# Kernel optimization log

Hardware: AMD Instinct MI355X
Metric: run time of the kernel (lower is better)

Reference implementation:

```python
import jax, jax.numpy as jnp
import numpy as np

N_NODES = 50000
N_EDGES = 1000000
IN_F = 128
OUT_F = 128
K = 4
NEG_SLOPE = 0.01  # torch nn.LeakyReLU() default
EPS = 1e-8


def setup_inputs() -> dict:
    key = jax.random.key(0)
    k1, k2, k3, k4, k5, k6 = jax.random.split(key, 6)
    x = jax.random.normal(k1, (N_NODES, IN_F), dtype=jnp.float32)
    e = jax.random.uniform(k2, (N_NODES, K), dtype=jnp.float32)
    stdv = 1.0 / np.sqrt(OUT_F)
    weights = jax.random.uniform(k3, (K, IN_F, OUT_F), minval=-stdv, maxval=stdv, dtype=jnp.float32)
    a = jax.random.normal(k4, (K, 2 * OUT_F, 1), dtype=jnp.float32) * 0.1
    # edge_index with no self-loops (remove_self_loops is then a no-op)
    row = jax.random.randint(k5, (N_EDGES,), 0, N_NODES)
    off = jax.random.randint(k6, (N_EDGES,), 1, N_NODES)
    col = (row + off) % N_NODES
    adj = jnp.stack([row, col]).astype(jnp.int64)
    return {"x": x, "e": e, "weights": weights, "a": a, "adj": adj}


def _canet_gat_forward(x, e, weights, a, adj):
    N = x.shape[0]
    out_f = weights.shape[-1]
    # add self loops (input has none)
    loops = jnp.arange(N, dtype=adj.dtype)
    src = jnp.concatenate([adj[0], loops])  # [Et]
    dst = jnp.concatenate([adj[1], loops])  # [Et]

    # per-head projection: [K, N, O]
    h = jnp.einsum('nd,kdo->kno', x, weights)

    # attention logits: a = [a_src; a_dst], logit_e = leakyrelu(h[src].a_src + h[dst].a_dst)
    a_src = a[:, :out_f, 0]   # [K, O]
    a_dst = a[:, out_f:, 0]   # [K, O]
    s_src = jnp.einsum('kno,ko->kn', h, a_src)  # [K, N]
    s_dst = jnp.einsum('kno,ko->kn', h, a_dst)  # [K, N]
    logits = s_src[:, src] + s_dst[:, dst]      # [K, Et]
    logits = jnp.where(logits >= 0, logits, NEG_SLOPE * logits)
    logits_max = jnp.max(logits, axis=1, keepdims=True)  # global max per head
    edge_e = jnp.exp(logits - logits_max)                # [K, Et]

    outputs = []
    for k in range(h.shape[0]):  # small fixed loop over heads (avoids [K,Et,O] blowup)
        denom = jax.ops.segment_sum(edge_e[k], src, num_segments=N) + EPS   # [N]
        msg = edge_e[k][:, None] * h[k][dst]                                # [Et, O]
        hi_k = jax.ops.segment_sum(msg, src, num_segments=N)                # [N, O]
        outputs.append(hi_k / denom[:, None])
    outputs = jnp.stack(outputs, axis=1)  # [N, K, O]

    out = jnp.sum(e[:, :, None] * outputs, axis=1)  # [N, O]
    return out + x  # residual (in_features == out_features)


def reference(x, e, weights, a, adj):
    return _canet_gat_forward(x, e, weights, a, adj)
```

## Files before the change

kernel.cpp:

```cpp
#include <hip/hip_runtime.h>
#include <hip/hip_bf16.h>
#include <cstddef>

#define NN 50000
#define NE 1000000
#define F  128
#define KH 4
#define NEG 0.01f
#define EPSF 1e-8f
#define CAP 64
#define NBIN 196
#define BINCAP 8192
#define EPB 4096
#define NB1 ((NE + EPB - 1) / EPB)
#define NBW 256
#define NBP 1024

typedef short bf16x8 __attribute__((ext_vector_type(8)));
typedef float f32x4 __attribute__((ext_vector_type(4)));

__device__ inline ushort f2bf(float f) {
    __hip_bfloat16 b = __float2bfloat16(f);
    return *reinterpret_cast<ushort*>(&b);
}
__device__ inline float2 bf2_to_f2(unsigned int v) {
    union { unsigned int u; float f; } a, b;
    a.u = (v & 0xffffu) << 16;
    b.u = v & 0xffff0000u;
    return make_float2(a.f, b.f);
}
__device__ inline unsigned int packbf(float xl, float xh) {
    return (unsigned int)f2bf(xl) | ((unsigned int)f2bf(xh) << 16);
}
__device__ inline float lk(float v) { return (v >= 0.f) ? v : NEG * v; }

__global__ __launch_bounds__(256) void bin_kernel(const int* __restrict__ adj,
                                                  int* __restrict__ binTail,
                                                  unsigned int* __restrict__ binbuf,
                                                  const float* __restrict__ W,
                                                  const float* __restrict__ a,
                                                  ushort* __restrict__ wt,
                                                  float* __restrict__ vvg) {
    int b = blockIdx.x;
    int tid = threadIdx.x;
    if (b < NB1) {
        __shared__ int hist[NBIN];
        __shared__ int rpos[NBIN];
        int base = b * EPB;
        int nloc = min(EPB, NE - base);
        for (int i = tid; i < NBIN; i += 256) hist[i] = 0;
        __syncthreads();
        unsigned int pk[16];
#pragma unroll
        for (int u = 0; u < 16; u++) {
            int off = u * 256 + tid;
            if (off < nloc) {
                int e = base + off;
                unsigned int s = (unsigned int)adj[e];
                unsigned int d = (unsigned int)adj[NE + e];
                pk[u] = (s << 16) | d;
                atomicAdd(&hist[s >> 8], 1);
            } else pk[u] = 0xffffffffu;
        }
        __syncthreads();
        for (int i = tid; i < NBIN; i += 256) rpos[i] = atomicAdd(&binTail[i], hist[i]);
        __syncthreads();
#pragma unroll
        for (int u = 0; u < 16; u++) {
            if (pk[u] != 0xffffffffu) {
                int bn = pk[u] >> 24;
                int p = atomicAdd(&rpos[bn], 1);
                if (p < BINCAP) binbuf[(size_t)bn * BINCAP + p] = pk[u];
            }
        }
    } else if (b < NB1 + NBW) {
        int i = (b - NB1) * 256 + tid;
        int k = i >> 14;
        int dd = (i >> 7) & 127;
        int o = i & 127;
        wt[((size_t)k * F + o) * F + dd] = f2bf(W[i]);
    } else {
        int j0 = tid * 4;
#pragma unroll
        for (int ii = 0; ii < 4; ii++) {
            int j = j0 + ii;
            int side = j >> 9;
            int k = (j >> 7) & 3;
            int dd = j & 127;
            const float4* Wr = (const float4*)(W + (size_t)k * F * F + (size_t)dd * F);
            const float4* ar = (const float4*)(a + (size_t)k * 2 * F + side * F);
            float acc = 0.f;
#pragma unroll 8
            for (int o = 0; o < F / 4; o++) {
                float4 wv = Wr[o], av = ar[o];
                acc += wv.x * av.x + wv.y * av.y + wv.z * av.z + wv.w * av.w;
            }
            vvg[j] = acc;
        }
    }
}

__global__ __launch_bounds__(256) void build_prep_kernel(const int* __restrict__ binTail,
                                                         const unsigned int* __restrict__ binbuf,
                                                         int* __restrict__ cnt,
                                                         ushort* __restrict__ bucket16,
                                                         const float* __restrict__ vvg,
                                                         const float* __restrict__ x,
                                                         unsigned int* __restrict__ xb2,
                                                         float* __restrict__ ssrc4,
                                                         float* __restrict__ sdst4,
                                                         int* __restrict__ mxsi) {
    int tid = threadIdx.x;
    __shared__ int lcnt[256];
    __shared__ __align__(16) ushort lbkt[256][CAP];
    __shared__ float vv_s[8][F];

    if (blockIdx.x < NBIN) {
        int b = blockIdx.x;
        lcnt[tid] = 0;
        __syncthreads();
        int tail = min(binTail[b], BINCAP);
        const unsigned int* bb = binbuf + (size_t)b * BINCAP;
        for (int i = tid; i < tail; i += 256) {
            unsigned int pk = bb[i];
            int sl = (pk >> 16) & 255;
            int p = atomicAdd(&lcnt[sl], 1);
            if (p < CAP) lbkt[sl][p] = (ushort)(pk & 0xffffu);
        }
        __syncthreads();
        int n0 = b << 8;
        cnt[n0 + tid] = lcnt[tid];
        uint4* dst = (uint4*)(bucket16 + (size_t)n0 * CAP);
        const uint4* src = (const uint4*)lbkt;
        for (int i = tid; i < 2048; i += 256) dst[i] = src[i];
        return;
    }

    ((float4*)vv_s)[tid] = ((const float4*)vvg)[tid];
    __syncthreads();

    int wv = tid >> 6, lane = tid & 63;
    int gw = (blockIdx.x - NBIN) * 4 + wv;
    const float2* x2 = (const float2*)x;
    float2 vs[4], vd[4];
#pragma unroll
    for (int k = 0; k < 4; k++) {
        vs[k] = *(const float2*)&vv_s[k][2 * lane];
        vd[k] = *(const float2*)&vv_s[4 + k][2 * lane];
    }
    int l1 = lane & 1, l2 = lane & 2, l4 = lane & 4;
    int j = 4 * l1 + l2 + (l4 >> 2);
    float* sp = (j < 4) ? (ssrc4 + j) : (sdst4 + (j - 4));
    float mxv = 0.f;

    for (int n = gw; n < NN; n += NBP * 4) {
        float2 xv = x2[(size_t)n * 64 + lane];
        xb2[(size_t)n * 64 + lane] = packbf(xv.x, xv.y);
        float s[8];
#pragma unroll
        for (int k = 0; k < 4; k++) {
            s[k]     = xv.x * vs[k].x + xv.y * vs[k].y;
            s[4 + k] = xv.x * vd[k].x + xv.y * vd[k].y;
        }
        float t[4], u[2], v;
#pragma unroll
        for (int i = 0; i < 4; i++) {
            float mine = l1 ? s[4 + i] : s[i];
            float oth  = __shfl_xor(l1 ? s[i] : s[4 + i], 1);
            t[i] = mine + oth;
        }
#pragma unroll
        for (int i = 0; i < 2; i++) {
            float mine = l2 ? t[2 + i] : t[i];
            float oth  = __shfl_xor(l2 ? t[i] : t[2 + i], 2);
            u[i] = mine + oth;
        }
        {
            float mine = l4 ? u[1] : u[0];
            float oth  = __shfl_xor(l4 ? u[0] : u[1], 4);
            v = mine + oth;
        }
        v += __shfl_xor(v, 8);
        v += __shfl_xor(v, 16);
        v += __shfl_xor(v, 32);
        if (lane < 8) sp[(size_t)n * 4] = v;
        mxv = fmaxf(mxv, v);
    }
    if (lane < 8) atomicMax(&mxsi[j], __float_as_int(mxv));
}

__global__ __launch_bounds__(256) void aggregate_kernel(const unsigned int* __restrict__ xb2,
                                                        const float* __restrict__ ssrc4,
                                                        const float* __restrict__ sdst4,
                                                        const float* __restrict__ mxs,
                                                        const int* __restrict__ cnt,
                                                        const ushort* __restrict__ bucket16,
                                                        const float* __restrict__ ew,
                                                        unsigned int* __restrict__ z2) {
    int wv = threadIdx.x >> 6, lane = threadIdx.x & 63;
    int n = blockIdx.x * 4 + wv;
    if (n >= NN) return;

    __shared__ int dsh[4][64];
    __shared__ __align__(16) float wsh[4][64][4];

    float4 mxa = *(const float4*)&mxs[0];
    float4 mxb = *(const float4*)&mxs[4];
    float m0 = lk(mxa.x + mxb.x), m1 = lk(mxa.y + mxb.y);
    float m2 = lk(mxa.z + mxb.z), m3 = lk(mxa.w + mxb.w);
    float4 ss  = *(const float4*)&ssrc4[(size_t)n * 4];
    float4 sdn = *(const float4*)&sdst4[(size_t)n * 4];
    float w0s = __expf(lk(ss.x + sdn.x) - m0);
    float w1s = __expf(lk(ss.y + sdn.y) - m1);
    float w2s = __expf(lk(ss.z + sdn.z) - m2);
    float w3s = __expf(lk(ss.w + sdn.w) - m3);

    int deg = min(cnt[n], CAP);
    if (lane < deg) {
        int d = (int)bucket16[(size_t)n * CAP + lane];
        dsh[wv][lane] = d;
        float4 sd = *(const float4*)&sdst4[(size_t)d * 4];
        float4 w;
        w.x = __expf(lk(ss.x + sd.x) - m0);
        w.y = __expf(lk(ss.y + sd.y) - m1);
        w.z = __expf(lk(ss.z + sd.z) - m2);
        w.w = __expf(lk(ss.w + sd.w) - m3);
        *(float4*)&wsh[wv][lane][0] = w;
    }

    float a0[4], a1[4], den[4];
    {
        float2 f = bf2_to_f2(xb2[(size_t)n * 64 + lane]);
        a0[0] = w0s * f.x; a1[0] = w0s * f.y; den[0] = w0s;
        a0[1] = w1s * f.x; a1[1] = w1s * f.y; den[1] = w1s;
        a0[2] = w2s * f.x; a1[2] = w2s * f.y; den[2] = w2s;
        a0[3] = w3s * f.x; a1[3] = w3s * f.y; den[3] = w3s;
    }

    for (int i = 0; i < deg; i += 8) {
        int du[8]; float4 wu[8]; unsigned int vu[8];
#pragma unroll
        for (int u = 0; u < 8; u++) {
            int iu = i + u;
            bool val = iu < deg;
            int sel = val ? iu : 0;
            du[u] = dsh[wv][sel];
            float4 w = *(const float4*)&wsh[wv][sel][0];
            wu[u] = val ? w : make_float4(0.f, 0.f, 0.f, 0.f);
        }
#pragma unroll
        for (int u = 0; u < 8; u++) vu[u] = xb2[(size_t)du[u] * 64 + lane];
#pragma unroll
        for (int u = 0; u < 8; u++) {
            float2 f = bf2_to_f2(vu[u]);
            float4 w = wu[u];
            a0[0] += w.x * f.x; a1[0] += w.x * f.y; den[0] += w.x;
            a0[1] += w.y * f.x; a1[1] += w.y * f.y; den[1] += w.y;
            a0[2] += w.z * f.x; a1[2] += w.z * f.y; den[2] += w.z;
            a0[3] += w.w * f.x; a1[3] += w.w * f.y; den[3] += w.w;
        }
    }

    float4 e4 = *(const float4*)&ew[(size_t)n * 4];
    float i0 = e4.x / (den[0] + EPSF);
    float i1 = e4.y / (den[1] + EPSF);
    float i2 = e4.z / (den[2] + EPSF);
    float i3 = e4.w / (den[3] + EPSF);
    size_t zb = (size_t)n * 256;
    z2[zb +   0 + lane] = packbf(a0[0] * i0, a1[0] * i0);
    z2[zb +  64 + lane] = packbf(a0[1] * i1, a1[1] * i1);
    z2[zb + 128 + lane] = packbf(a0[2] * i2, a1[2] * i2);
    z2[zb + 192 + lane] = packbf(a0[3] * i3, a1[3] * i3);
}

#define MT 64
__global__ __launch_bounds__(256) void gemm2_kernel(const ushort* __restrict__ z,
                                                    const ushort* __restrict__ wt,
                                                    const float* __restrict__ x,
                                                    float* __restrict__ out) {
    int row0 = blockIdx.x * MT;
    int tid = threadIdx.x;
    int wave = tid >> 6, lane = tid & 63;
    int quad = lane >> 4, l16 = lane & 15;
    __shared__ ushort ws[F][136];

    int arow = row0 + wave * 16 + l16;
    if (arow >= NN) arow = NN - 1;

    f32x4 acc[8];
#pragma unroll
    for (int i = 0; i < 8; i++) acc[i] = (f32x4){0.f, 0.f, 0.f, 0.f};

    for (int k = 0; k < KH; k++) {
        __syncthreads();
        const ushort* wk = wt + (size_t)k * F * F;
        for (int i = tid; i < F * 16; i += 256) {
            int r = i >> 4, c = (i & 15) * 8;
            *(uint4*)&ws[r][c] = *(const uint4*)&wk[r * F + c];
        }
        __syncthreads();
#pragma unroll
        for (int kt = 0; kt < 4; kt++) {
            int kb = kt * 32 + quad * 8;
            bf16x8 af = *(const bf16x8*)&z[(size_t)arow * 512 + k * F + kb];
#pragma unroll
            for (int ni = 0; ni < 8; ni++) {
                bf16x8 bf = *(const bf16x8*)&ws[ni * 16 + l16][kb];
                acc[ni] = __builtin_amdgcn_mfma_f32_16x16x32_bf16(af, bf, acc[ni], 0, 0, 0);
            }
        }
    }
#pragma unroll
    for (int r = 0; r < 4; r++) {
        int n = row0 + wave * 16 + quad * 4 + r;
        if (n < NN) {
#pragma unroll
            for (int ni = 0; ni < 8; ni++) {
                int o = ni * 16 + l16;
                out[(size_t)n * F + o] = x[(size_t)n * F + o] + acc[ni][r];
            }
        }
    }
}

extern "C" void kernel_launch(void* const* d_in, const int* in_sizes, int n_in,
                              void* d_out, int out_size, void* d_ws, size_t ws_size,
                              hipStream_t stream) {
    const float* x = (const float*)d_in[0];
    const float* e = (const float*)d_in[1];
    const float* W = (const float*)d_in[2];
    const float* a = (const float*)d_in[3];
    const int*   adj = (const int*)d_in[4];
    float* out = (float*)d_out;

    char* ws = (char*)d_ws;
    auto take = [&](size_t bytes) {
        char* p = ws;
        ws += (bytes + 255) & ~(size_t)255;
        return p;
    };
    ushort* z      = (ushort*)take((size_t)NN * KH * F * sizeof(ushort));
    unsigned int* xb2 = (unsigned int*)take((size_t)NN * F * sizeof(ushort));
    ushort* wt     = (ushort*)take((size_t)KH * F * F * sizeof(ushort));
    float* ssrc4   = (float*)take((size_t)NN * 4 * sizeof(float));
    float* sdst4   = (float*)take((size_t)NN * 4 * sizeof(float));
    int*   cnt     = (int*)take((size_t)NBIN * 256 * sizeof(int));
    ushort* bucket16 = (ushort*)take((size_t)NBIN * 256 * CAP * sizeof(ushort));
    unsigned int* binbuf = (unsigned int*)take((size_t)NBIN * BINCAP * sizeof(unsigned int));
    int*   binTail = (int*)take((size_t)NBIN * sizeof(int) + 32);
    float* mxs     = (float*)(binTail + NBIN);
    float* vvg     = (float*)take((size_t)8 * F * sizeof(float));

    hipMemsetAsync(binTail, 0, (size_t)NBIN * sizeof(int) + 32, stream);
    bin_kernel<<<NB1 + NBW + 1, 256, 0, stream>>>(adj, binTail, binbuf, W, a, wt, vvg);
    build_prep_kernel<<<NBIN + NBP, 256, 0, stream>>>(binTail, binbuf, cnt, bucket16,
                                                      vvg, x, xb2, ssrc4, sdst4, (int*)mxs);
    aggregate_kernel<<<(NN + 3) / 4, 256, 0, stream>>>(xb2, ssrc4, sdst4, mxs, cnt,
                                                       bucket16, e, (unsigned int*)z);
    gemm2_kernel<<<(NN + MT - 1) / MT, 256, 0, stream>>>(z, wt, x, out);
}
```

Measured before the change: 239.7 us.

## Shrink build_prep LDS footprint, double prep blocks, process two nodes per iteration

The bin-build path no longer stages a 256xCAP ushort bucket in shared memory. It counts in a first pass, then re-reads the bin and scatters edge ids directly to the global bucket using a second atomic position counter. This cuts shared memory per block from about 37KB to 4KB, which should raise occupancy. The score path doubles its block count (NBP) and handles two nodes per loop iteration so loads and shuffles can overlap. In exchange, the bin is read twice and the global writes are scattered 2-byte stores instead of coalesced 16-byte copies.

```diff
diff --git a/kernel.cpp b/kernel.cpp
--- a/kernel.cpp
+++ b/kernel.cpp
@@ -14,7 +14,8 @@
 #define EPB 4096
 #define NB1 ((NE + EPB - 1) / EPB)
 #define NBW 256
-#define NBP 1024
+#define NBP 2048
+#define STR (NBP * 4)
 
 typedef short bf16x8 __attribute__((ext_vector_type(8)));
 typedef float f32x4 __attribute__((ext_vector_type(4)));
@@ -111,32 +112,35 @@
                                                          float* __restrict__ sdst4,
                                                          int* __restrict__ mxsi) {
     int tid = threadIdx.x;
-    __shared__ int lcnt[256];
-    __shared__ __align__(16) ushort lbkt[256][CAP];
-    __shared__ float vv_s[8][F];
+    __shared__ __align__(16) int shmem[1024];
 
     if (blockIdx.x < NBIN) {
         int b = blockIdx.x;
+        int* lcnt = shmem;
+        int* lpos = shmem + 256;
         lcnt[tid] = 0;
+        lpos[tid] = 0;
         __syncthreads();
         int tail = min(binTail[b], BINCAP);
         const unsigned int* bb = binbuf + (size_t)b * BINCAP;
         for (int i = tid; i < tail; i += 256) {
             unsigned int pk = bb[i];
-            int sl = (pk >> 16) & 255;
-            int p = atomicAdd(&lcnt[sl], 1);
-            if (p < CAP) lbkt[sl][p] = (ushort)(pk & 0xffffu);
+            atomicAdd(&lcnt[(pk >> 16) & 255], 1);
         }
         __syncthreads();
         int n0 = b << 8;
         cnt[n0 + tid] = lcnt[tid];
-        uint4* dst = (uint4*)(bucket16 + (size_t)n0 * CAP);
-        const uint4* src = (const uint4*)lbkt;
-        for (int i = tid; i < 2048; i += 256) dst[i] = src[i];
+        for (int i = tid; i < tail; i += 256) {
+            unsigned int pk = bb[i];
+            int sl = (pk >> 16) & 255;
+            int p = atomicAdd(&lpos[sl], 1);
+            if (p < CAP) bucket16[(size_t)(n0 + sl) * CAP + p] = (ushort)(pk & 0xffffu);
+        }
         return;
     }
 
-    ((float4*)vv_s)[tid] = ((const float4*)vvg)[tid];
+    float* vvf = (float*)shmem;
+    ((float4*)vvf)[tid] = ((const float4*)vvg)[tid];
     __syncthreads();
 
     int wv = tid >> 6, lane = tid & 63;
@@ -145,46 +149,66 @@
     float2 vs[4], vd[4];
 #pragma unroll
     for (int k = 0; k < 4; k++) {
-        vs[k] = *(const float2*)&vv_s[k][2 * lane];
-        vd[k] = *(const float2*)&vv_s[4 + k][2 * lane];
+        vs[k] = *(const float2*)&vvf[k * F + 2 * lane];
+        vd[k] = *(const float2*)&vvf[(4 + k) * F + 2 * lane];
     }
     int l1 = lane & 1, l2 = lane & 2, l4 = lane & 4;
     int j = 4 * l1 + l2 + (l4 >> 2);
     float* sp = (j < 4) ? (ssrc4 + j) : (sdst4 + (j - 4));
     float mxv = 0.f;
 
-    for (int n = gw; n < NN; n += NBP * 4) {
-        float2 xv = x2[(size_t)n * 64 + lane];
-        xb2[(size_t)n * 64 + lane] = packbf(xv.x, xv.y);
-        float s[8];
+    for (int n = gw; n < NN; n += 2 * STR) {
+        int nb = n + STR;
+        bool vb = nb < NN;
+        float2 xa = x2[(size_t)n * 64 + lane];
+        float2 xbv = vb ? x2[(size_t)nb * 64 + lane] : make_float2(0.f, 0.f);
+        xb2[(size_t)n * 64 + lane] = packbf(xa.x, xa.y);
+        if (vb) xb2[(size_t)nb * 64 + lane] = packbf(xbv.x, xbv.y);
+        float s[8], q[8];
 #pragma unroll
         for (int k = 0; k < 4; k++) {
-            s[k]     = xv.x * vs[k].x + xv.y * vs[k].y;
-            s[4 + k] = xv.x * vd[k].x + xv.y * vd[k].y;
-        }
-        float t[4], u[2], v;
+            s[k]     = xa.x * vs[k].x + xa.y * vs[k].y;
+            s[4 + k] = xa.x * vd[k].x + xa.y * vd[k].y;
+            q[k]     = xbv.x * vs[k].x + xbv.y * vs[k].y;
+            q[4 + k] = xbv.x * vd[k].x + xbv.y * vd[k].y;
+        }
+        float tA[4], tB[4];
 #pragma unroll
         for (int i = 0; i < 4; i++) {
-            float mine = l1 ? s[4 + i] : s[i];
-            float oth  = __shfl_xor(l1 ? s[i] : s[4 + i], 1);
-            t[i] = mine + oth;
-        }
+            float mA = l1 ? s[4 + i] : s[i];
+            float oA = __shfl_xor(l1 ? s[i] : s[4 + i], 1);
+            tA[i] = mA + oA;
+            float mB = l1 ? q[4 + i] : q[i];
+            float oB = __shfl_xor(l1 ? q[i] : q[4 + i], 1);
+            tB[i] = mB + oB;
+        }
+        float uA[2], uB[2];
 #pragma unroll
         for (int i = 0; i < 2; i++) {
-            float mine = l2 ? t[2 + i] : t[i];
-            float oth  = __shfl_xor(l2 ? t[i] : t[2 + i], 2);
-            u[i] = mine + oth;
-        }
+            float mA = l2 ? tA[2 + i] : tA[i];
+            float oA = __shfl_xor(l2 ? tA[i] : tA[2 + i], 2);
+            uA[i] = mA + oA;
+            float mB = l2 ? tB[2 + i] : tB[i];
+            float oB = __shfl_xor(l2 ? tB[i] : tB[2 + i], 2);
+            uB[i] = mB + oB;
+        }
+        float vA, vB;
         {
-            float mine = l4 ? u[1] : u[0];
-            float oth  = __shfl_xor(l4 ? u[0] : u[1], 4);
-            v = mine + oth;
-        }
-        v += __shfl_xor(v, 8);
-        v += __shfl_xor(v, 16);
-        v += __shfl_xor(v, 32);
-        if (lane < 8) sp[(size_t)n * 4] = v;
-        mxv = fmaxf(mxv, v);
+            float mA = l4 ? uA[1] : uA[0];
+            float oA = __shfl_xor(l4 ? uA[0] : uA[1], 4);
+            vA = mA + oA;
+            float mB = l4 ? uB[1] : uB[0];
+            float oB = __shfl_xor(l4 ? uB[0] : uB[1], 4);
+            vB = mB + oB;
+        }
+        vA += __shfl_xor(vA, 8);  vB += __shfl_xor(vB, 8);
+        vA += __shfl_xor(vA, 16); vB += __shfl_xor(vB, 16);
+        vA += __shfl_xor(vA, 32); vB += __shfl_xor(vB, 32);
+        if (lane < 8) {
+            sp[(size_t)n * 4] = vA;
+            if (vb) sp[(size_t)nb * 4] = vB;
+        }
+        mxv = fmaxf(mxv, fmaxf(vA, vB));
     }
     if (lane < 8) atomicMax(&mxsi[j], __float_as_int(mxv));
 }
```

After: 286.9 us. 19.7% more time.
